# Optimization experiments

Hardware: AMD Instinct MI355X
Metric: run time of the kernel (lower is better)

## Reference

```python
import jax, jax.numpy as jnp
import numpy as np

NUM_NODES = 100000
D = 256            # node_hidden_dim
H = 256            # edge_hidden_dim
P = 524288         # num_pairs


def setup_inputs() -> dict:
    key = jax.random.key(0)
    k1, k2, k3, k4, k5, k6 = jax.random.split(key, 6)
    h_nodes = jax.random.normal(k1, (NUM_NODES, D), dtype=jnp.float32)
    dst = jax.random.randint(k2, (P,), 0, NUM_NODES, dtype=jnp.int64)
    src = jax.random.randint(k3, (P,), 0, NUM_NODES, dtype=jnp.int64)
    # Bias-free MLP weights, stored as [in, out] so forward is x @ W
    s1 = 1.0 / np.sqrt(2 * D)
    s2 = 1.0 / np.sqrt(H)
    W1 = jax.random.uniform(k4, (2 * D, H), jnp.float32, -s1, s1)
    W2 = jax.random.uniform(k5, (H, H), jnp.float32, -s2, s2)
    W3 = jax.random.uniform(k6, (H, 2), jnp.float32, -s2, s2)
    return {"h_nodes": h_nodes, "dst": dst, "src": src, "W1": W1, "W2": W2, "W3": W3}


def reference(h_nodes, dst, src, W1, W2, W3):
    # gather src/dst embeddings and concat -> [P, 2D]
    h_pair = jnp.concatenate([h_nodes[dst], h_nodes[src]], axis=-1)
    x = jax.nn.relu(h_pair @ W1)   # [P, H]
    x = jax.nn.relu(x @ W2)        # [P, H]
    return x @ W3                  # [P, 2] edge logits
```

## Files before the change

kernel.cpp:

```cpp
#include <hip/hip_runtime.h>
#include <stdint.h>

typedef __attribute__((ext_vector_type(8))) short short8;
typedef __attribute__((ext_vector_type(4))) short short4v;
typedef __attribute__((ext_vector_type(4))) float floatx4;

__device__ __forceinline__ unsigned short f2bf(float x) {
  unsigned int u = __float_as_uint(x);
  u += 0x7fffu + ((u >> 16) & 1u);
  return (unsigned short)(u >> 16);
}
__device__ __forceinline__ float bf2f(unsigned short b) {
  return __uint_as_float(((unsigned int)b) << 16);
}
__device__ __forceinline__ int sw3(int r) { return (r & 7) ^ (((r >> 3) & 1) * 3); }

__global__ void prep_kernel(const float* __restrict__ h, const float* __restrict__ W1,
                            const float* __restrict__ W2, const float* __restrict__ W3,
                            unsigned short* __restrict__ HBF, unsigned short* __restrict__ W1F,
                            unsigned short* __restrict__ W2F, unsigned short* __restrict__ W3F,
                            int nh4) {
  const int t = threadIdx.x;
  int b = blockIdx.x;
  if (b < 512) {
    int u = b * 256 + t;
    int j = u & 7, kq = (u >> 3) & 3, n = (u >> 5) & 255, k32 = u >> 13;
    W1F[u] = f2bf(W1[(k32 * 32 + kq * 8 + j) * 256 + n]);
    return;
  }
  b -= 512;
  if (b < 256) {
    int u = b * 256 + t;
    int j = u & 7, kq = (u >> 3) & 3, n = (u >> 5) & 255, k32 = u >> 13;
    W2F[u] = f2bf(W2[(k32 * 32 + kq * 8 + j) * 256 + n]);
    return;
  }
  b -= 256;
  if (b < 16) {
    int u = b * 256 + t;
    int j = u & 7, L = (u >> 3) & 63, k32 = u >> 9;
    int n = L & 15, kq = L >> 4;
    W3F[u] = (n < 2) ? f2bf(W3[(k32 * 32 + kq * 8 + j) * 2 + n]) : (unsigned short)0;
    return;
  }
  b -= 16;
  int u = b * 256 + t;
  if (u < nh4) {
    float4 v = ((const float4*)h)[u];
    short4v s;
    s[0] = (short)f2bf(v.x); s[1] = (short)f2bf(v.y);
    s[2] = (short)f2bf(v.z); s[3] = (short)f2bf(v.w);
    ((short4v*)HBF)[u] = s;
  }
}

__global__ __launch_bounds__(256, 2)
void edge_mlp3(const unsigned short* __restrict__ hbf,
               const int* __restrict__ dst,
               const int* __restrict__ src,
               const unsigned short* __restrict__ W1F,
               const unsigned short* __restrict__ W2F,
               const unsigned short* __restrict__ W3F,
               float* __restrict__ out) {
  __shared__ unsigned short A[64 * 512];
  __shared__ int ioff[128];
  unsigned short* X  = A;
  unsigned short* X2 = A + 16384;

  const int t = threadIdx.x, lane = t & 63, w = t >> 6;
  const int lq = lane >> 4, lm = lane & 15;
  const int m0 = blockIdx.x * 64;

  if (t < 64)       ioff[t] = dst[m0 + t];
  else if (t < 128) ioff[t] = src[m0 + t - 64];
  __syncthreads();

  {
    const int c = lane, half = (c >= 32) ? 64 : 0, cc = c & 31;
    short8 g[16];
#pragma unroll
    for (int it = 0; it < 16; ++it) {
      int node = ioff[half + it * 4 + w];
      g[it] = ((const short8*)hbf)[node * 32 + cc];
    }
#pragma unroll
    for (int it = 0; it < 16; ++it) {
      int r = it * 4 + w;
      *(short8*)&A[r * 512 + ((c ^ sw3(r)) << 3)] = g[it];
    }
  }

  floatx4 acc[4][4];
#pragma unroll
  for (int i = 0; i < 4; ++i)
#pragma unroll
    for (int j = 0; j < 4; ++j) acc[i][j] = (floatx4)(0.0f);
  __syncthreads();

  const short8* B1 = (const short8*)W1F;
  const short8* B2 = (const short8*)W2F;

  {
    short8 bq[4][4];
#pragma unroll
    for (int s = 0; s < 4; ++s)
#pragma unroll
      for (int jt = 0; jt < 4; ++jt)
        bq[s][jt] = B1[(s * 256 + w * 64 + jt * 16 + lm) * 4 + lq];

#pragma unroll
    for (int s = 0; s < 16; ++s) {
#pragma unroll
      for (int i = 0; i < 4; ++i) {
        int r = i * 16 + lm, cch = s * 4 + lq;
        short8 af = *(const short8*)&A[r * 512 + ((cch ^ sw3(r)) << 3)];
#pragma unroll
        for (int j = 0; j < 4; ++j)
          acc[i][j] = __builtin_amdgcn_mfma_f32_16x16x32_bf16(af, bq[s & 3][j], acc[i][j], 0, 0, 0);
      }
      if (s < 12)
#pragma unroll
        for (int jt = 0; jt < 4; ++jt)
          bq[s & 3][jt] = B1[((s + 4) * 256 + w * 64 + jt * 16 + lm) * 4 + lq];
    }
  }
  __syncthreads();
#pragma unroll
  for (int i = 0; i < 4; ++i) {
    int row0 = i * 16 + lq * 4;
#pragma unroll
    for (int j = 0; j < 4; ++j) {
      int col = w * 64 + j * 16 + lm, c8 = col >> 3, ce = col & 7;
#pragma unroll
      for (int rg = 0; rg < 4; ++rg) {
        int row = row0 + rg;
        float v = acc[i][j][rg];
        v = v > 0.0f ? v : 0.0f;
        X[row * 256 + (((c8 ^ sw3(row)) << 3) | ce)] = f2bf(v);
      }
    }
  }
#pragma unroll
  for (int i = 0; i < 4; ++i)
#pragma unroll
    for (int j = 0; j < 4; ++j) acc[i][j] = (floatx4)(0.0f);
  __syncthreads();

  {
    short8 bq[4][4];
#pragma unroll
    for (int s = 0; s < 4; ++s)
#pragma unroll
      for (int jt = 0; jt < 4; ++jt)
        bq[s][jt] = B2[(s * 256 + w * 64 + jt * 16 + lm) * 4 + lq];

#pragma unroll
    for (int s = 0; s < 8; ++s) {
#pragma unroll
      for (int i = 0; i < 4; ++i) {
        int r = i * 16 + lm, cch = s * 4 + lq;
        short8 af = *(const short8*)&X[r * 256 + ((cch ^ sw3(r)) << 3)];
#pragma unroll
        for (int j = 0; j < 4; ++j)
          acc[i][j] = __builtin_amdgcn_mfma_f32_16x16x32_bf16(af, bq[s & 3][j], acc[i][j], 0, 0, 0);
      }
      if (s < 4)
#pragma unroll
        for (int jt = 0; jt < 4; ++jt)
          bq[s & 3][jt] = B2[((s + 4) * 256 + w * 64 + jt * 16 + lm) * 4 + lq];
    }
  }
  __syncthreads();
#pragma unroll
  for (int i = 0; i < 4; ++i) {
    int row0 = i * 16 + lq * 4;
#pragma unroll
    for (int j = 0; j < 4; ++j) {
      int col = w * 64 + j * 16 + lm, c8 = col >> 3, ce = col & 7;
#pragma unroll
      for (int rg = 0; rg < 4; ++rg) {
        int row = row0 + rg;
        float v = acc[i][j][rg];
        v = v > 0.0f ? v : 0.0f;
        X2[row * 256 + (((c8 ^ sw3(row)) << 3) | ce)] = f2bf(v);
      }
    }
  }
  __syncthreads();

  {
    floatx4 a3 = (floatx4)(0.0f);
    const short8* B3 = (const short8*)W3F;
#pragma unroll
    for (int s = 0; s < 8; ++s) {
      short8 b3 = B3[s * 64 + lane];
      int r = w * 16 + lm, cch = s * 4 + lq;
      short8 af = *(const short8*)&X2[r * 256 + ((cch ^ sw3(r)) << 3)];
      a3 = __builtin_amdgcn_mfma_f32_16x16x32_bf16(af, b3, a3, 0, 0, 0);
    }
    if (lm < 2) {
#pragma unroll
      for (int rg = 0; rg < 4; ++rg)
        out[(m0 + w * 16 + lq * 4 + rg) * 2 + lm] = a3[rg];
    }
  }
}

__global__ void wfrag_kernel(const float* __restrict__ W,
                             unsigned short* __restrict__ out, int total) {
  int u = blockIdx.x * 256 + threadIdx.x;
  if (u >= total) return;
  int j = u & 7, kq = (u >> 3) & 3, n = (u >> 5) & 255, k32 = u >> 13;
  out[u] = f2bf(W[(k32 * 32 + kq * 8 + j) * 256 + n]);
}

__global__ __launch_bounds__(256, 2)
void edge_mlp_fb(const float* __restrict__ h,
                 const int* __restrict__ dst,
                 const int* __restrict__ src,
                 const unsigned short* __restrict__ W1F,
                 const unsigned short* __restrict__ W2F,
                 const float* __restrict__ W3,
                 float* __restrict__ out) {
  __shared__ unsigned short A[64 * 512];
  __shared__ float w3s[512];
  __shared__ int ioff[128];
  unsigned short* X = A;
  const int t = threadIdx.x, lane = t & 63, w = t >> 6;
  const int lq = lane >> 4, lm = lane & 15;
  const int m0 = blockIdx.x * 64;
  if (t < 64) ioff[t] = dst[m0 + t];
  else if (t < 128) ioff[t] = src[m0 + t - 64];
  w3s[t] = W3[t];
  w3s[t + 256] = W3[t + 256];
  __syncthreads();
  {
    const int c = lane, half = (c >= 32) ? 64 : 0, cc = c & 31;
#pragma unroll
    for (int it = 0; it < 16; ++it) {
      int r = it * 4 + w;
      int node = ioff[half + r];
      const float4* h4 = (const float4*)h;
      float4 v0 = h4[node * 64 + cc * 2], v1 = h4[node * 64 + cc * 2 + 1];
      short8 v;
      v[0] = (short)f2bf(v0.x); v[1] = (short)f2bf(v0.y);
      v[2] = (short)f2bf(v0.z); v[3] = (short)f2bf(v0.w);
      v[4] = (short)f2bf(v1.x); v[5] = (short)f2bf(v1.y);
      v[6] = (short)f2bf(v1.z); v[7] = (short)f2bf(v1.w);
      *(short8*)&A[r * 512 + ((c ^ (r & 7)) << 3)] = v;
    }
  }
  floatx4 acc[4][4];
#pragma unroll
  for (int i = 0; i < 4; ++i)
#pragma unroll
    for (int j = 0; j < 4; ++j) acc[i][j] = (floatx4)(0.0f);
  __syncthreads();
  const short8* B1 = (const short8*)W1F;
  const short8* B2 = (const short8*)W2F;
#pragma unroll
  for (int k32 = 0; k32 < 16; ++k32) {
    short8 b[4], af[4];
#pragma unroll
    for (int jt = 0; jt < 4; ++jt)
      b[jt] = B1[(k32 * 256 + w * 64 + jt * 16 + lm) * 4 + lq];
#pragma unroll
    for (int i = 0; i < 4; ++i) {
      int r = i * 16 + lm, c = k32 * 4 + lq;
      af[i] = *(const short8*)&A[r * 512 + ((c ^ (r & 7)) << 3)];
    }
#pragma unroll
    for (int i = 0; i < 4; ++i)
#pragma unroll
      for (int j = 0; j < 4; ++j)
        acc[i][j] = __builtin_amdgcn_mfma_f32_16x16x32_bf16(af[i], b[j], acc[i][j], 0, 0, 0);
  }
  __syncthreads();
#pragma unroll
  for (int i = 0; i < 4; ++i) {
    int row0 = i * 16 + lq * 4;
#pragma unroll
    for (int j = 0; j < 4; ++j) {
      int col = w * 64 + j * 16 + lm, c8 = col >> 3, ce = col & 7;
#pragma unroll
      for (int rg = 0; rg < 4; ++rg) {
        int row = row0 + rg;
        float v = acc[i][j][rg];
        v = v > 0.0f ? v : 0.0f;
        X[row * 256 + (((c8 ^ (row & 7)) << 3) | ce)] = f2bf(v);
      }
    }
  }
#pragma unroll
  for (int i = 0; i < 4; ++i)
#pragma unroll
    for (int j = 0; j < 4; ++j) acc[i][j] = (floatx4)(0.0f);
  __syncthreads();
#pragma unroll
  for (int k32 = 0; k32 < 8; ++k32) {
    short8 b[4], af[4];
#pragma unroll
    for (int jt = 0; jt < 4; ++jt)
      b[jt] = B2[(k32 * 256 + w * 64 + jt * 16 + lm) * 4 + lq];
#pragma unroll
    for (int i = 0; i < 4; ++i) {
      int r = i * 16 + lm, c = k32 * 4 + lq;
      af[i] = *(const short8*)&X[r * 256 + ((c ^ (r & 7)) << 3)];
    }
#pragma unroll
    for (int i = 0; i < 4; ++i)
#pragma unroll
      for (int j = 0; j < 4; ++j)
        acc[i][j] = __builtin_amdgcn_mfma_f32_16x16x32_bf16(af[i], b[j], acc[i][j], 0, 0, 0);
  }
  __syncthreads();
#pragma unroll
  for (int i = 0; i < 4; ++i) {
    int row0 = i * 16 + lq * 4;
#pragma unroll
    for (int j = 0; j < 4; ++j) {
      int col = w * 64 + j * 16 + lm, c8 = col >> 3, ce = col & 7;
#pragma unroll
      for (int rg = 0; rg < 4; ++rg) {
        int row = row0 + rg;
        float v = acc[i][j][rg];
        v = v > 0.0f ? v : 0.0f;
        X[row * 256 + (((c8 ^ (row & 7)) << 3) | ce)] = f2bf(v);
      }
    }
  }
  __syncthreads();
  {
    int r = t >> 2, o = (t >> 1) & 1, hh = t & 1;
    float s = 0.0f;
#pragma unroll
    for (int it = 0; it < 16; ++it) {
      int c = hh * 16 + it;
      short8 xv = *(const short8*)&X[r * 256 + ((c ^ (r & 7)) << 3)];
#pragma unroll
      for (int e = 0; e < 8; ++e)
        s += bf2f((unsigned short)xv[e]) * w3s[((c << 3) + e) * 2 + o];
    }
    s += __shfl_xor(s, 1);
    if (hh == 0) out[(m0 + r) * 2 + o] = s;
  }
}

extern "C" void kernel_launch(void* const* d_in, const int* in_sizes, int n_in,
                              void* d_out, int out_size, void* d_ws, size_t ws_size,
                              hipStream_t stream) {
  const float* h   = (const float*)d_in[0];
  const int*   dst = (const int*)d_in[1];
  const int*   src = (const int*)d_in[2];
  const float* W1  = (const float*)d_in[3];
  const float* W2  = (const float*)d_in[4];
  const float* W3  = (const float*)d_in[5];
  float* out = (float*)d_out;

  const int h_elems = in_sizes[0];
  const int n_pairs = in_sizes[1];
  const int ntiles  = n_pairs / 64;

  const size_t hbf_elems = (size_t)h_elems;
  const bool use_hbf =
      ws_size >= (hbf_elems + 131072 + 65536 + 4096) * sizeof(unsigned short);

  unsigned short* HBF = (unsigned short*)d_ws;
  unsigned short* W1F = HBF + hbf_elems;
  unsigned short* W2F = W1F + 131072;
  unsigned short* W3F = W2F + 65536;

  if (use_hbf) {
    int nh4 = h_elems / 4;
    int grid = 512 + 256 + 16 + (nh4 + 255) / 256;
    prep_kernel<<<grid, 256, 0, stream>>>(h, W1, W2, W3, HBF, W1F, W2F, W3F, nh4);
    edge_mlp3<<<ntiles, 256, 0, stream>>>(HBF, dst, src, W1F, W2F, W3F, out);
  } else {
    unsigned short* W1Fb = (unsigned short*)d_ws;
    unsigned short* W2Fb = W1Fb + 131072;
    wfrag_kernel<<<512, 256, 0, stream>>>(W1, W1Fb, 131072);
    wfrag_kernel<<<256, 256, 0, stream>>>(W2, W2Fb, 65536);
    edge_mlp_fb<<<ntiles, 256, 0, stream>>>(h, dst, src, W1Fb, W2Fb, W3, out);
  }
}
```

Measured before the change: 410.2 us.

## Halve LDS tile, gather via global_load_lds in two phases, raise occupancy

The edge MLP kernel now stages the dst and src halves of the 64x512 concatenated input separately into a single 64x256 LDS buffer. Each half is loaded with global_load_lds (direct global-to-LDS) and followed by its half of the first GEMM K-loop. The layer-2 and layer-3 activations reuse the same buffer, and the B-fragment prefetch depth drops from 4 to 2 stages, so launch bounds rise from 2 to 4 blocks per CU. The prep kernel converts 8 floats per thread instead of 4. In exchange, the gather and compute phases no longer overlap within a block, and the shallower prefetch may expose more weight-load latency.

```diff
diff --git a/kernel.cpp b/kernel.cpp
--- a/kernel.cpp
+++ b/kernel.cpp
@@ -15,11 +15,17 @@
 }
 __device__ __forceinline__ int sw3(int r) { return (r & 7) ^ (((r >> 3) & 1) * 3); }
 
+__device__ __forceinline__ void gld16(const unsigned short* g, unsigned short* l) {
+  __builtin_amdgcn_global_load_lds(
+      (const __attribute__((address_space(1))) void*)g,
+      (__attribute__((address_space(3))) void*)l, 16, 0, 0);
+}
+
 __global__ void prep_kernel(const float* __restrict__ h, const float* __restrict__ W1,
                             const float* __restrict__ W2, const float* __restrict__ W3,
                             unsigned short* __restrict__ HBF, unsigned short* __restrict__ W1F,
                             unsigned short* __restrict__ W2F, unsigned short* __restrict__ W3F,
-                            int nh4) {
+                            int nh8) {
   const int t = threadIdx.x;
   int b = blockIdx.x;
   if (b < 512) {
@@ -45,16 +51,19 @@
   }
   b -= 16;
   int u = b * 256 + t;
-  if (u < nh4) {
-    float4 v = ((const float4*)h)[u];
-    short4v s;
-    s[0] = (short)f2bf(v.x); s[1] = (short)f2bf(v.y);
-    s[2] = (short)f2bf(v.z); s[3] = (short)f2bf(v.w);
-    ((short4v*)HBF)[u] = s;
-  }
-}
-
-__global__ __launch_bounds__(256, 2)
+  if (u < nh8) {
+    const float4* h4 = (const float4*)h;
+    float4 v0 = h4[u * 2], v1 = h4[u * 2 + 1];
+    short8 s;
+    s[0] = (short)f2bf(v0.x); s[1] = (short)f2bf(v0.y);
+    s[2] = (short)f2bf(v0.z); s[3] = (short)f2bf(v0.w);
+    s[4] = (short)f2bf(v1.x); s[5] = (short)f2bf(v1.y);
+    s[6] = (short)f2bf(v1.z); s[7] = (short)f2bf(v1.w);
+    ((short8*)HBF)[u] = s;
+  }
+}
+
+__global__ __launch_bounds__(256, 4)
 void edge_mlp3(const unsigned short* __restrict__ hbf,
                const int* __restrict__ dst,
                const int* __restrict__ src,
@@ -62,69 +71,91 @@
                const unsigned short* __restrict__ W2F,
                const unsigned short* __restrict__ W3F,
                float* __restrict__ out) {
-  __shared__ unsigned short A[64 * 512];
+  __shared__ __align__(16) unsigned short A[64 * 256];
   __shared__ int ioff[128];
-  unsigned short* X  = A;
-  unsigned short* X2 = A + 16384;
 
   const int t = threadIdx.x, lane = t & 63, w = t >> 6;
   const int lq = lane >> 4, lm = lane & 15;
   const int m0 = blockIdx.x * 64;
+  const int mm = lane & 31, rh = lane >> 5, rbase = w * 16;
 
   if (t < 64)       ioff[t] = dst[m0 + t];
   else if (t < 128) ioff[t] = src[m0 + t - 64];
   __syncthreads();
 
-  {
-    const int c = lane, half = (c >= 32) ? 64 : 0, cc = c & 31;
-    short8 g[16];
-#pragma unroll
-    for (int it = 0; it < 16; ++it) {
-      int node = ioff[half + it * 4 + w];
-      g[it] = ((const short8*)hbf)[node * 32 + cc];
-    }
-#pragma unroll
-    for (int it = 0; it < 16; ++it) {
-      int r = it * 4 + w;
-      *(short8*)&A[r * 512 + ((c ^ sw3(r)) << 3)] = g[it];
-    }
-  }
-
   floatx4 acc[4][4];
 #pragma unroll
   for (int i = 0; i < 4; ++i)
 #pragma unroll
     for (int j = 0; j < 4; ++j) acc[i][j] = (floatx4)(0.0f);
-  __syncthreads();
 
   const short8* B1 = (const short8*)W1F;
   const short8* B2 = (const short8*)W2F;
 
-  {
-    short8 bq[4][4];
-#pragma unroll
-    for (int s = 0; s < 4; ++s)
-#pragma unroll
-      for (int jt = 0; jt < 4; ++jt)
-        bq[s][jt] = B1[(s * 256 + w * 64 + jt * 16 + lm) * 4 + lq];
-
-#pragma unroll
-    for (int s = 0; s < 16; ++s) {
+#pragma unroll
+  for (int tt = 0; tt < 8; ++tt) {
+    int rl = rbase + 2 * tt + rh;
+    int node = ioff[rl];
+    gld16(hbf + (size_t)node * 256 + ((mm ^ sw3(rl)) << 3), &A[(rbase + 2 * tt) * 256]);
+  }
+  __syncthreads();
+
+  {
+    short8 bq[2][4];
+#pragma unroll
+    for (int jt = 0; jt < 4; ++jt) bq[0][jt] = B1[(0 * 256 + w * 64 + jt * 16 + lm) * 4 + lq];
+#pragma unroll
+    for (int jt = 0; jt < 4; ++jt) bq[1][jt] = B1[(1 * 256 + w * 64 + jt * 16 + lm) * 4 + lq];
+#pragma unroll
+    for (int s = 0; s < 8; ++s) {
 #pragma unroll
       for (int i = 0; i < 4; ++i) {
-        int r = i * 16 + lm, cch = s * 4 + lq;
-        short8 af = *(const short8*)&A[r * 512 + ((cch ^ sw3(r)) << 3)];
+        int r = i * 16 + lm, c = s * 4 + lq;
+        short8 af = *(const short8*)&A[r * 256 + ((c ^ sw3(r)) << 3)];
 #pragma unroll
         for (int j = 0; j < 4; ++j)
-          acc[i][j] = __builtin_amdgcn_mfma_f32_16x16x32_bf16(af, bq[s & 3][j], acc[i][j], 0, 0, 0);
-      }
-      if (s < 12)
+          acc[i][j] = __builtin_amdgcn_mfma_f32_16x16x32_bf16(af, bq[s & 1][j], acc[i][j], 0, 0, 0);
+      }
+      if (s < 6)
 #pragma unroll
         for (int jt = 0; jt < 4; ++jt)
-          bq[s & 3][jt] = B1[((s + 4) * 256 + w * 64 + jt * 16 + lm) * 4 + lq];
-    }
-  }
-  __syncthreads();
+          bq[s & 1][jt] = B1[((s + 2) * 256 + w * 64 + jt * 16 + lm) * 4 + lq];
+    }
+  }
+  __syncthreads();
+
+#pragma unroll
+  for (int tt = 0; tt < 8; ++tt) {
+    int rl = rbase + 2 * tt + rh;
+    int node = ioff[64 + rl];
+    gld16(hbf + (size_t)node * 256 + ((mm ^ sw3(rl)) << 3), &A[(rbase + 2 * tt) * 256]);
+  }
+  __syncthreads();
+
+  {
+    short8 bq[2][4];
+#pragma unroll
+    for (int jt = 0; jt < 4; ++jt) bq[0][jt] = B1[(8 * 256 + w * 64 + jt * 16 + lm) * 4 + lq];
+#pragma unroll
+    for (int jt = 0; jt < 4; ++jt) bq[1][jt] = B1[(9 * 256 + w * 64 + jt * 16 + lm) * 4 + lq];
+#pragma unroll
+    for (int s = 0; s < 8; ++s) {
+#pragma unroll
+      for (int i = 0; i < 4; ++i) {
+        int r = i * 16 + lm, c = s * 4 + lq;
+        short8 af = *(const short8*)&A[r * 256 + ((c ^ sw3(r)) << 3)];
+#pragma unroll
+        for (int j = 0; j < 4; ++j)
+          acc[i][j] = __builtin_amdgcn_mfma_f32_16x16x32_bf16(af, bq[s & 1][j], acc[i][j], 0, 0, 0);
+      }
+      if (s < 6)
+#pragma unroll
+        for (int jt = 0; jt < 4; ++jt)
+          bq[s & 1][jt] = B1[((s + 10) * 256 + w * 64 + jt * 16 + lm) * 4 + lq];
+    }
+  }
+  __syncthreads();
+
 #pragma unroll
   for (int i = 0; i < 4; ++i) {
     int row0 = i * 16 + lq * 4;
@@ -136,7 +167,7 @@
         int row = row0 + rg;
         float v = acc[i][j][rg];
         v = v > 0.0f ? v : 0.0f;
-        X[row * 256 + (((c8 ^ sw3(row)) << 3) | ce)] = f2bf(v);
+        A[row * 256 + (((c8 ^ sw3(row)) << 3) | ce)] = f2bf(v);
       }
     }
   }
@@ -147,30 +178,29 @@
   __syncthreads();
 
   {
-    short8 bq[4][4];
-#pragma unroll
-    for (int s = 0; s < 4; ++s)
-#pragma unroll
-      for (int jt = 0; jt < 4; ++jt)
-        bq[s][jt] = B2[(s * 256 + w * 64 + jt * 16 + lm) * 4 + lq];
-
+    short8 bq[2][4];
+#pragma unroll
+    for (int jt = 0; jt < 4; ++jt) bq[0][jt] = B2[(0 * 256 + w * 64 + jt * 16 + lm) * 4 + lq];
+#pragma unroll
+    for (int jt = 0; jt < 4; ++jt) bq[1][jt] = B2[(1 * 256 + w * 64 + jt * 16 + lm) * 4 + lq];
 #pragma unroll
     for (int s = 0; s < 8; ++s) {
 #pragma unroll
       for (int i = 0; i < 4; ++i) {
-        int r = i * 16 + lm, cch = s * 4 + lq;
-        short8 af = *(const short8*)&X[r * 256 + ((cch ^ sw3(r)) << 3)];
+        int r = i * 16 + lm, c = s * 4 + lq;
+        short8 af = *(const short8*)&A[r * 256 + ((c ^ sw3(r)) << 3)];
 #pragma unroll
         for (int j = 0; j < 4; ++j)
-          acc[i][j] = __builtin_amdgcn_mfma_f32_16x16x32_bf16(af, bq[s & 3][j], acc[i][j], 0, 0, 0);
-      }
-      if (s < 4)
+          acc[i][j] = __builtin_amdgcn_mfma_f32_16x16x32_bf16(af, bq[s & 1][j], acc[i][j], 0, 0, 0);
+      }
+      if (s < 6)
 #pragma unroll
         for (int jt = 0; jt < 4; ++jt)
-          bq[s & 3][jt] = B2[((s + 4) * 256 + w * 64 + jt * 16 + lm) * 4 + lq];
-    }
-  }
-  __syncthreads();
+          bq[s & 1][jt] = B2[((s + 2) * 256 + w * 64 + jt * 16 + lm) * 4 + lq];
+    }
+  }
+  __syncthreads();
+
 #pragma unroll
   for (int i = 0; i < 4; ++i) {
     int row0 = i * 16 + lq * 4;
@@ -182,7 +212,7 @@
         int row = row0 + rg;
         float v = acc[i][j][rg];
         v = v > 0.0f ? v : 0.0f;
-        X2[row * 256 + (((c8 ^ sw3(row)) << 3) | ce)] = f2bf(v);
+        A[row * 256 + (((c8 ^ sw3(row)) << 3) | ce)] = f2bf(v);
       }
     }
   }
@@ -195,7 +225,7 @@
     for (int s = 0; s < 8; ++s) {
       short8 b3 = B3[s * 64 + lane];
       int r = w * 16 + lm, cch = s * 4 + lq;
-      short8 af = *(const short8*)&X2[r * 256 + ((cch ^ sw3(r)) << 3)];
+      short8 af = *(const short8*)&A[r * 256 + ((cch ^ sw3(r)) << 3)];
       a3 = __builtin_amdgcn_mfma_f32_16x16x32_bf16(af, b3, a3, 0, 0, 0);
     }
     if (lm < 2) {
@@ -371,9 +401,9 @@
   unsigned short* W3F = W2F + 65536;
 
   if (use_hbf) {
-    int nh4 = h_elems / 4;
-    int grid = 512 + 256 + 16 + (nh4 + 255) / 256;
-    prep_kernel<<<grid, 256, 0, stream>>>(h, W1, W2, W3, HBF, W1F, W2F, W3F, nh4);
+    int nh8 = h_elems / 8;
+    int grid = 512 + 256 + 16 + (nh8 + 255) / 256;
+    prep_kernel<<<grid, 256, 0, stream>>>(h, W1, W2, W3, HBF, W1F, W2F, W3F, nh8);
     edge_mlp3<<<ntiles, 256, 0, stream>>>(HBF, dst, src, W1F, W2F, W3F, out);
   } else {
     unsigned short* W1Fb = (unsigned short*)d_ws;
```

After: 556.1 us. +35.6%, slower.
